# Kernel tuning notes

Measured on AMD Instinct MI355X. Metric: run time of the kernel, lower is better.

Reference implementation:

```python
import jax, jax.numpy as jnp
import numpy as np

B, S, F, D, H, L = 32768, 32, 10, 64, 4, 2
HD = D // H  # head_dim = 16
DFF = 2 * D  # ffn hidden = 128
DH = D // 2  # head hidden = 32


def _ln(x, g, b, eps=1e-5):
    mu = jnp.mean(x, axis=-1, keepdims=True)
    var = jnp.mean((x - mu) ** 2, axis=-1, keepdims=True)
    return (x - mu) * jax.lax.rsqrt(var + eps) * g + b


def setup_inputs() -> dict:
    key = jax.random.key(0)
    ks = jax.random.split(key, 16)
    r = lambda k, shp, s=0.05: jax.random.normal(k, shp, dtype=jnp.float32) * s
    return {
        "x": jax.random.normal(ks[0], (B, S, F), dtype=jnp.float32),
        "w_in": r(ks[1], (F, D)), "b_in": jnp.zeros((D,), jnp.float32),
        "pos": r(ks[2], (S, D)),
        "wq": r(ks[3], (L, D, D)), "wk": r(ks[4], (L, D, D)), "wv": r(ks[5], (L, D, D)),
        "wo": r(ks[6], (L, D, D)), "bo": jnp.zeros((L, D), jnp.float32),
        "g1": jnp.ones((L, D), jnp.float32), "be1": jnp.zeros((L, D), jnp.float32),
        "g2": jnp.ones((L, D), jnp.float32), "be2": jnp.zeros((L, D), jnp.float32),
        "w1": r(ks[7], (L, D, DFF)), "b1": jnp.zeros((L, DFF), jnp.float32),
        "w2": r(ks[8], (L, DFF, D)), "b2": jnp.zeros((L, D), jnp.float32),
        "hw1": r(ks[9], (D, DH)), "hb1": jnp.zeros((DH,), jnp.float32),
        "hw2": r(ks[10], (DH, 1)), "hb2": jnp.zeros((1,), jnp.float32),
    }


def reference(x, w_in, b_in, pos, wq, wk, wv, wo, bo, g1, be1, g2, be2,
              w1, b1, w2, b2, hw1, hb1, hw2, hb2):
    b, s, _ = x.shape
    h = x @ w_in + b_in + pos[None, :s]  # [B,S,D]
    scale = 1.0 / np.sqrt(HD)
    for i in range(L):
        # --- attention sublayer (pre-LN) ---
        hn = _ln(h, g1[i], be1[i])
        q = (hn @ wq[i]).reshape(b, s, H, HD)
        k = (hn @ wk[i]).reshape(b, s, H, HD)
        v = (hn @ wv[i]).reshape(b, s, H, HD)
        scores = jnp.einsum('bqhd,bkhd->bhqk', q, k) * scale
        attn = jax.nn.softmax(scores, axis=-1)
        ctx = jnp.einsum('bhqk,bkhd->bqhd', attn, v).reshape(b, s, D)
        h = h + ctx @ wo[i] + bo[i]
        # --- FFN sublayer (pre-LN) ---
        hn = _ln(h, g2[i], be2[i])
        h = h + jax.nn.relu(hn @ w1[i] + b1[i]) @ w2[i] + b2[i]
    pooled = h.mean(axis=1)  # [B,D]
    out = jax.nn.relu(pooled @ hw1 + hb1) @ hw2 + hb2
    return jnp.tanh(out)  # [B,1]
```

## Files before the change

### kernel.cpp

```cpp
#include <hip/hip_runtime.h>
#include <cmath>

typedef _Float16 h8_t __attribute__((ext_vector_type(8)));
typedef float f4_t __attribute__((ext_vector_type(4)));

constexpr int Bsz = 32768, S = 32, F = 10, Dm = 64, Ln = 2, DFF = 128;
constexpr int ZP = 72;
constexpr int VP = 40;
constexpr int NB = 2;

constexpr int ZONE_H = S * ZP;
constexpr int VT_H   = Dm * VP;
constexpr int SMEM_H = NB * (ZONE_H + VT_H);

constexpr int NFRAG = 4 + Ln * 64;
constexpr size_t PB_OFF = (size_t)NFRAG * 512 * 2;

__global__ __launch_bounds__(256, 2)
void prep_kernel(const float* __restrict__ w_in, const float* __restrict__ b_in,
                 const float* __restrict__ pos,
                 const float* __restrict__ wq, const float* __restrict__ wk,
                 const float* __restrict__ wv, const float* __restrict__ wo,
                 const float* __restrict__ w1, const float* __restrict__ w2,
                 _Float16* __restrict__ wsf, float* __restrict__ pbf) {
  int gid = blockIdx.x * 256 + threadIdx.x;
  int lane = gid & 63;
  int l15 = lane & 15, lk8 = (lane >> 4) << 3;
  if (gid < NFRAG * 64) {
    int frag = gid >> 6;
    float vals[8];
    if (frag < 4) {
      int n = 16 * frag + l15;
      #pragma unroll
      for (int j = 0; j < 8; ++j) {
        int k = lk8 + j;
        vals[j] = (k < F) ? w_in[k * Dm + n] : 0.f;
      }
    } else {
      int f = frag - 4;
      int layer = f >> 6; f &= 63;
      const float* W; int ncols, n, kbase;
      if (f < 32) {
        int sub = f >> 3, g = f & 7;
        int nt = g & 3, kt = g >> 2;
        W = ((sub == 0) ? wk : (sub == 1) ? wv : (sub == 2) ? wq : wo) + layer * Dm * Dm;
        ncols = Dm; n = 16 * nt + l15; kbase = kt * 32 + lk8;
      } else if (f < 48) {
        int g = f - 32, nt = g & 7, kt = g >> 3;
        W = w1 + layer * Dm * DFF; ncols = DFF; n = 16 * nt + l15; kbase = kt * 32 + lk8;
      } else {
        int g = f - 48, nt = g & 3, kt = g >> 2;
        W = w2 + layer * DFF * Dm; ncols = Dm; n = 16 * nt + l15; kbase = kt * 32 + lk8;
      }
      #pragma unroll
      for (int j = 0; j < 8; ++j) vals[j] = W[(kbase + j) * ncols + n];
    }
    h8_t o;
    #pragma unroll
    for (int j = 0; j < 8; ++j) o[j] = (_Float16)vals[j];
    *(h8_t*)&wsf[(size_t)gid * 8] = o;
  } else if (gid < NFRAG * 64 + 8 * 64) {
    int r = gid - NFRAG * 64;
    int pb = r >> 6;
    int mt = pb >> 2, nt = pb & 3;
    int row = 16 * mt + ((lane >> 4) << 2);
    int col = 16 * nt + l15;
    f4_t v;
    #pragma unroll
    for (int q = 0; q < 4; ++q) v[q] = pos[(row + q) * Dm + col] + b_in[col];
    *(f4_t*)&pbf[(size_t)r * 4] = v;
  }
}

__global__ __launch_bounds__(128, 4)
void tlob_kernel(const float* __restrict__ x,
                 const float* __restrict__ g1, const float* __restrict__ be1,
                 const float* __restrict__ g2, const float* __restrict__ be2,
                 const float* __restrict__ bo, const float* __restrict__ b1,
                 const float* __restrict__ b2, const float* __restrict__ hw1,
                 const float* __restrict__ hb1, const float* __restrict__ hw2,
                 const float* __restrict__ hb2,
                 const _Float16* __restrict__ wsf, const float* __restrict__ pbf,
                 float* __restrict__ out) {
  __shared__ __align__(16) _Float16 smem[SMEM_H];
  const int tid = threadIdx.x;
  const int lane = tid & 63;
  const int wid = tid >> 6;
  const int elem = blockIdx.x * NB + wid;

  _Float16* zone = smem + wid * ZONE_H;
  _Float16* vT = smem + NB * ZONE_H + wid * VT_H;

  const int l15 = lane & 15;
  const int G = lane >> 4;
  const int lk8 = G << 3;
  const int r0b = G << 2;
  const int swzR = ((l15 >> 2) & 3) << 3;
  int col4[4];
  #pragma unroll
  for (int nt = 0; nt < 4; ++nt) col4[nt] = l15 + 16 * nt;

  const h8_t* FR = (const h8_t*)wsf;
  auto ldf = [&](int f) -> h8_t { return FR[f * 64 + lane]; };

  f4_t z4; z4[0] = 0.f; z4[1] = 0.f; z4[2] = 0.f; z4[3] = 0.f;
  h8_t hz;
  #pragma unroll
  for (int j = 0; j < 8; ++j) hz[j] = (_Float16)0.f;

  auto mfma = [&](h8_t a, h8_t b, f4_t c) -> f4_t {
    return __builtin_amdgcn_mfma_f32_16x16x32_f16(a, b, c, 0, 0, 0);
  };
  auto cstore = [&](_Float16* buf, int pitch, int mt, int col, f4_t v, float scale) {
    int c = col ^ lk8;
    int r = 16 * mt + r0b;
    #pragma unroll
    for (int q = 0; q < 4; ++q) buf[(r + q) * pitch + c] = (_Float16)(v[q] * scale);
  };
  auto zfrag = [&](int i1, int i2) -> h8_t {
    return *(const h8_t*)&zone[(l15 + 16 * i1) * ZP + ((i2 * 32 + lk8) ^ swzR)];
  };

  h8_t xa[2];
  #pragma unroll
  for (int mt = 0; mt < 2; ++mt) {
    const float* xr = x + (size_t)elem * (S * F) + (16 * mt + l15) * F;
    h8_t v = hz;
    #pragma unroll
    for (int j = 0; j < 8; ++j) {
      int f = lk8 + j;
      if (f < F) v[j] = (_Float16)xr[f];
    }
    xa[mt] = v;
  }

  f4_t hacc[2][4];
  #pragma unroll
  for (int nt = 0; nt < 4; ++nt) {
    h8_t wb = ldf(nt);
    #pragma unroll
    for (int mt = 0; mt < 2; ++mt) {
      f4_t ini = *(const f4_t*)&pbf[((size_t)(mt * 4 + nt) * 64 + lane) * 4];
      hacc[mt][nt] = mfma(xa[mt], wb, ini);
    }
  }

  auto doLN = [&](const float* g, const float* be, h8_t fr[2][2]) {
    float gv[4], bv[4];
    #pragma unroll
    for (int nt = 0; nt < 4; ++nt) { gv[nt] = g[col4[nt]]; bv[nt] = be[col4[nt]]; }
    #pragma unroll
    for (int mt = 0; mt < 2; ++mt) {
      f4_t ps = hacc[mt][0] + hacc[mt][1] + hacc[mt][2] + hacc[mt][3];
      f4_t pq = hacc[mt][0] * hacc[mt][0] + hacc[mt][1] * hacc[mt][1] +
                hacc[mt][2] * hacc[mt][2] + hacc[mt][3] * hacc[mt][3];
      #pragma unroll
      for (int m = 1; m <= 8; m <<= 1) {
        #pragma unroll
        for (int q = 0; q < 4; ++q) {
          ps[q] += __shfl_xor(ps[q], m);
          pq[q] += __shfl_xor(pq[q], m);
        }
      }
      f4_t muv, rsv;
      #pragma unroll
      for (int q = 0; q < 4; ++q) {
        float mu = ps[q] * (1.f / 64.f);
        float var = pq[q] * (1.f / 64.f) - mu * mu;
        muv[q] = mu; rsv[q] = rsqrtf(var + 1e-5f);
      }
      #pragma unroll
      for (int nt = 0; nt < 4; ++nt) {
        int c = col4[nt] ^ lk8;
        int r = 16 * mt + r0b;
        #pragma unroll
        for (int q = 0; q < 4; ++q) {
          float hn = (hacc[mt][nt][q] - muv[q]) * rsv[q] * gv[nt] + bv[nt];
          zone[(r + q) * ZP + c] = (_Float16)hn;
        }
      }
    }
    #pragma unroll
    for (int i1 = 0; i1 < 2; ++i1)
      #pragma unroll
      for (int i2 = 0; i2 < 2; ++i2) fr[i1][i2] = zfrag(i1, i2);
  };

  #pragma unroll 1
  for (int layer = 0; layer < Ln; ++layer) {
    const int fb = 4 + layer * 64;
    float bov[4];
    #pragma unroll
    for (int nt = 0; nt < 4; ++nt) bov[nt] = bo[layer * Dm + col4[nt]];

    h8_t hnf[2][2];
    doLN(g1 + layer * Dm, be1 + layer * Dm, hnf);

    h8_t kA[2][2];
    {
      #pragma unroll
      for (int nt = 0; nt < 4; ++nt) {
        h8_t w0 = ldf(fb + 0 + 0 * 4 + nt), w1f = ldf(fb + 0 + 1 * 4 + nt);
        #pragma unroll
        for (int mt = 0; mt < 2; ++mt) {
          f4_t acc = mfma(hnf[mt][0], w0, z4);
          acc = mfma(hnf[mt][1], w1f, acc);
          cstore(zone, ZP, mt, col4[nt], acc, 1.f);
        }
      }
      #pragma unroll
      for (int i1 = 0; i1 < 2; ++i1)
        #pragma unroll
        for (int i2 = 0; i2 < 2; ++i2) kA[i1][i2] = zfrag(i1, i2);
    }

    #pragma unroll
    for (int mtd = 0; mtd < 4; ++mtd) {
      h8_t a0 = ldf(fb + 8 + 0 * 4 + mtd), a1 = ldf(fb + 8 + 1 * 4 + mtd);
      #pragma unroll
      for (int nts = 0; nts < 2; ++nts) {
        f4_t acc = mfma(a0, hnf[nts][0], z4);
        acc = mfma(a1, hnf[nts][1], acc);
        cstore(vT, VP, mtd, l15 + 16 * nts, acc, 1.f);
      }
    }

    h8_t qf[2][2];
    {
      #pragma unroll
      for (int nt = 0; nt < 4; ++nt) {
        h8_t w0 = ldf(fb + 16 + 0 * 4 + nt), w1f = ldf(fb + 16 + 1 * 4 + nt);
        #pragma unroll
        for (int mt = 0; mt < 2; ++mt) {
          f4_t acc = mfma(hnf[mt][0], w0, z4);
          acc = mfma(hnf[mt][1], w1f, acc);
          cstore(zone, ZP, mt, col4[nt], acc, 0.25f);
        }
      }
      #pragma unroll
      for (int i1 = 0; i1 < 2; ++i1)
        #pragma unroll
        for (int i2 = 0; i2 < 2; ++i2) qf[i1][i2] = zfrag(i1, i2);
    }

    f4_t ctxf[2][4];
    #pragma unroll
    for (int hd = 0; hd < 4; ++hd) {
      const int kt = hd >> 1;
      bool keep = ((hd & 1) == 0) ? (lane < 32) : (lane >= 32);
      h8_t a0 = keep ? kA[0][kt] : hz;
      h8_t a1 = keep ? kA[1][kt] : hz;
      f4_t p[2][2];
      #pragma unroll
      for (int nq = 0; nq < 2; ++nq) {
        p[0][nq] = mfma(a0, qf[nq][kt], z4);
        p[1][nq] = mfma(a1, qf[nq][kt], z4);
      }
      #pragma unroll
      for (int nq = 0; nq < 2; ++nq) {
        #pragma unroll
        for (int mk = 0; mk < 2; ++mk)
          #pragma unroll
          for (int q = 0; q < 4; ++q) p[mk][nq][q] = __expf(p[mk][nq][q]);
        f4_t s4 = p[0][nq] + p[1][nq];
        float sm = s4[0] + s4[1] + s4[2] + s4[3];
        sm += __shfl_xor(sm, 16);
        sm += __shfl_xor(sm, 32);
        float inv = __builtin_amdgcn_rcpf(sm);
        #pragma unroll
        for (int mk = 0; mk < 2; ++mk)
          #pragma unroll
          for (int q = 0; q < 4; ++q) p[mk][nq][q] *= inv;
      }
      #pragma unroll
      for (int nq = 0; nq < 2; ++nq)
        #pragma unroll
        for (int mk = 0; mk < 2; ++mk)
          #pragma unroll
          for (int q = 0; q < 4; ++q)
            zone[(16 * nq + l15) * ZP + ((16 * mk + r0b + q) ^ swzR)] =
                (_Float16)p[mk][nq][q];
      h8_t pA0 = zfrag(0, 0), pA1 = zfrag(1, 0);
      h8_t vB = *(const h8_t*)&vT[(hd * 16 + l15) * VP + (lk8 ^ swzR)];
      ctxf[0][hd] = mfma(pA0, vB, z4);
      ctxf[1][hd] = mfma(pA1, vB, z4);
    }

    #pragma unroll
    for (int mt = 0; mt < 2; ++mt)
      #pragma unroll
      for (int hd = 0; hd < 4; ++hd) cstore(zone, ZP, mt, col4[hd], ctxf[mt][hd], 1.f);
    h8_t ca[2][2];
    #pragma unroll
    for (int i1 = 0; i1 < 2; ++i1)
      #pragma unroll
      for (int i2 = 0; i2 < 2; ++i2) ca[i1][i2] = zfrag(i1, i2);
    #pragma unroll
    for (int nt = 0; nt < 4; ++nt) {
      h8_t w0 = ldf(fb + 24 + 0 * 4 + nt), w1f = ldf(fb + 24 + 1 * 4 + nt);
      #pragma unroll
      for (int mt = 0; mt < 2; ++mt) {
        f4_t acc = mfma(ca[mt][0], w0, hacc[mt][nt]);
        acc = mfma(ca[mt][1], w1f, acc);
        #pragma unroll
        for (int q = 0; q < 4; ++q) hacc[mt][nt][q] = acc[q] + bov[nt];
      }
    }

    h8_t hn2f[2][2];
    doLN(g2 + layer * Dm, be2 + layer * Dm, hn2f);
    #pragma unroll 1
    for (int hf = 0; hf < 2; ++hf) {
      #pragma unroll
      for (int ntl = 0; ntl < 4; ++ntl) {
        int ntg = hf * 4 + ntl;
        h8_t w0 = ldf(fb + 32 + 0 * 8 + ntg), w1f = ldf(fb + 32 + 1 * 8 + ntg);
        float b1v = b1[layer * DFF + hf * 64 + col4[ntl]];
        f4_t bb; bb[0] = b1v; bb[1] = b1v; bb[2] = b1v; bb[3] = b1v;
        #pragma unroll
        for (int mt = 0; mt < 2; ++mt) {
          f4_t acc = mfma(hn2f[mt][0], w0, bb);
          acc = mfma(hn2f[mt][1], w1f, acc);
          #pragma unroll
          for (int q = 0; q < 4; ++q) acc[q] = fmaxf(acc[q], 0.f);
          cstore(zone, ZP, mt, col4[ntl], acc, 1.f);
        }
      }
      h8_t rf[2][2];
      #pragma unroll
      for (int i1 = 0; i1 < 2; ++i1)
        #pragma unroll
        for (int i2 = 0; i2 < 2; ++i2) rf[i1][i2] = zfrag(i1, i2);
      #pragma unroll
      for (int nt = 0; nt < 4; ++nt) {
        h8_t w0 = ldf(fb + 48 + (hf * 2 + 0) * 4 + nt);
        h8_t w1f = ldf(fb + 48 + (hf * 2 + 1) * 4 + nt);
        #pragma unroll
        for (int mt = 0; mt < 2; ++mt) {
          f4_t acc = mfma(rf[mt][0], w0, hacc[mt][nt]);
          hacc[mt][nt] = mfma(rf[mt][1], w1f, acc);
        }
      }
    }
    #pragma unroll
    for (int mt = 0; mt < 2; ++mt)
      #pragma unroll
      for (int nt = 0; nt < 4; ++nt) {
        float b2v = b2[layer * Dm + col4[nt]];
        #pragma unroll
        for (int q = 0; q < 4; ++q) hacc[mt][nt][q] += b2v;
      }
  }

  {
    float* pf = (float*)zone;
    #pragma unroll
    for (int nt = 0; nt < 4; ++nt) {
      float s = 0.f;
      #pragma unroll
      for (int mt = 0; mt < 2; ++mt)
        #pragma unroll
        for (int q = 0; q < 4; ++q) s += hacc[mt][nt][q];
      s += __shfl_xor(s, 16);
      s += __shfl_xor(s, 32);
      pf[col4[nt]] = s * (1.f / 32.f);
    }
    int j = lane & 31;
    float r = hb1[j];
    #pragma unroll
    for (int dd = 0; dd < 64; ++dd) r = fmaf(pf[dd], hw1[dd * 32 + j], r);
    r = fmaxf(r, 0.f);
    float t = r * hw2[j];
    t += __shfl_xor(t, 1); t += __shfl_xor(t, 2); t += __shfl_xor(t, 4);
    t += __shfl_xor(t, 8); t += __shfl_xor(t, 16);
    if (lane == 0) out[elem] = tanhf(t + hb2[0]);
  }
}

extern "C" void kernel_launch(void* const* d_in, const int* in_sizes, int n_in,
                              void* d_out, int out_size, void* d_ws, size_t ws_size,
                              hipStream_t stream) {
  (void)in_sizes; (void)n_in; (void)ws_size; (void)out_size;
  const float* x    = (const float*)d_in[0];
  const float* w_in = (const float*)d_in[1];
  const float* b_in = (const float*)d_in[2];
  const float* pos  = (const float*)d_in[3];
  const float* wq   = (const float*)d_in[4];
  const float* wk   = (const float*)d_in[5];
  const float* wv   = (const float*)d_in[6];
  const float* wo   = (const float*)d_in[7];
  const float* bo   = (const float*)d_in[8];
  const float* g1   = (const float*)d_in[9];
  const float* be1  = (const float*)d_in[10];
  const float* g2   = (const float*)d_in[11];
  const float* be2  = (const float*)d_in[12];
  const float* w1   = (const float*)d_in[13];
  const float* b1   = (const float*)d_in[14];
  const float* w2   = (const float*)d_in[15];
  const float* b2   = (const float*)d_in[16];
  const float* hw1  = (const float*)d_in[17];
  const float* hb1  = (const float*)d_in[18];
  const float* hw2  = (const float*)d_in[19];
  const float* hb2  = (const float*)d_in[20];
  float* out = (float*)d_out;

  _Float16* wsf = (_Float16*)d_ws;
  float* pbf = (float*)((char*)d_ws + PB_OFF);

  hipLaunchKernelGGL(prep_kernel, dim3(35), dim3(256), 0, stream,
                     w_in, b_in, pos, wq, wk, wv, wo, w1, w2, wsf, pbf);
  hipLaunchKernelGGL(tlob_kernel, dim3(Bsz / NB), dim3(128), 0, stream,
                     x, g1, be1, g2, be2, bo, b1, b2, hw1, hb1, hw2, hb2,
                     (const _Float16*)wsf, (const float*)pbf, out);
}
```

Before: 564.5 us.

## Stream attention heads from shared memory and store context per head to cut registers

Attention no longer keeps the Q fragments and all four heads' context accumulators in registers. Q fragments are read from shared memory per key tile, and each head's context goes straight to shared memory. Probabilities are staged in a separate per-wave buffer so they no longer overwrite Q in the zone. Lambdas become forceinline device functions, and launch bounds drop from 4 to 3 blocks per CU, presumably to relieve register pressure and spilling at the cost of fewer resident waves.

```diff
diff --git a/kernel.cpp b/kernel.cpp
--- a/kernel.cpp
+++ b/kernel.cpp
@@ -11,7 +11,8 @@
 
 constexpr int ZONE_H = S * ZP;
 constexpr int VT_H   = Dm * VP;
-constexpr int SMEM_H = NB * (ZONE_H + VT_H);
+constexpr int PB_H   = S * VP;
+constexpr int SMEM_H = NB * (ZONE_H + VT_H + PB_H);
 
 constexpr int NFRAG = 4 + Ln * 64;
 constexpr size_t PB_OFF = (size_t)NFRAG * 512 * 2;
@@ -72,7 +73,75 @@
   }
 }
 
-__global__ __launch_bounds__(128, 4)
+__device__ __forceinline__ f4_t mfma16(h8_t a, h8_t b, f4_t c) {
+  return __builtin_amdgcn_mfma_f32_16x16x32_f16(a, b, c, 0, 0, 0);
+}
+__device__ __forceinline__ void cstore(_Float16* buf, int pitch, int mt, int col,
+                                       f4_t v, float scale, int lk8, int r0b) {
+  int c = col ^ lk8;
+  int r = 16 * mt + r0b;
+  #pragma unroll
+  for (int q = 0; q < 4; ++q) buf[(r + q) * pitch + c] = (_Float16)(v[q] * scale);
+}
+__device__ __forceinline__ h8_t zfrag(const _Float16* zone, int i1, int i2,
+                                      int l15, int lk8, int swzR) {
+  return *(const h8_t*)&zone[(l15 + 16 * i1) * ZP + ((i2 * 32 + lk8) ^ swzR)];
+}
+__device__ __forceinline__ h8_t vpfrag(const _Float16* buf, int row,
+                                       int lk8, int swzR) {
+  return *(const h8_t*)&buf[row * VP + (lk8 ^ swzR)];
+}
+
+struct Frag22 { h8_t f[2][2]; };
+
+__device__ __forceinline__ Frag22 doLN(const f4_t (&hacc)[2][4],
+                                       const float* __restrict__ g,
+                                       const float* __restrict__ be,
+                                       _Float16* zone, int l15, int lk8,
+                                       int r0b, int swzR) {
+  float gv[4], bv[4];
+  #pragma unroll
+  for (int nt = 0; nt < 4; ++nt) { gv[nt] = g[l15 + 16 * nt]; bv[nt] = be[l15 + 16 * nt]; }
+  #pragma unroll
+  for (int mt = 0; mt < 2; ++mt) {
+    f4_t ps = hacc[mt][0] + hacc[mt][1] + hacc[mt][2] + hacc[mt][3];
+    f4_t pq = hacc[mt][0] * hacc[mt][0] + hacc[mt][1] * hacc[mt][1] +
+              hacc[mt][2] * hacc[mt][2] + hacc[mt][3] * hacc[mt][3];
+    #pragma unroll
+    for (int m = 1; m <= 8; m <<= 1) {
+      #pragma unroll
+      for (int q = 0; q < 4; ++q) {
+        ps[q] += __shfl_xor(ps[q], m);
+        pq[q] += __shfl_xor(pq[q], m);
+      }
+    }
+    f4_t muv, rsv;
+    #pragma unroll
+    for (int q = 0; q < 4; ++q) {
+      float mu = ps[q] * (1.f / 64.f);
+      float var = pq[q] * (1.f / 64.f) - mu * mu;
+      muv[q] = mu; rsv[q] = rsqrtf(var + 1e-5f);
+    }
+    #pragma unroll
+    for (int nt = 0; nt < 4; ++nt) {
+      int c = (l15 + 16 * nt) ^ lk8;
+      int r = 16 * mt + r0b;
+      #pragma unroll
+      for (int q = 0; q < 4; ++q) {
+        float hn = (hacc[mt][nt][q] - muv[q]) * rsv[q] * gv[nt] + bv[nt];
+        zone[(r + q) * ZP + c] = (_Float16)hn;
+      }
+    }
+  }
+  Frag22 out;
+  #pragma unroll
+  for (int i1 = 0; i1 < 2; ++i1)
+    #pragma unroll
+    for (int i2 = 0; i2 < 2; ++i2) out.f[i1][i2] = zfrag(zone, i1, i2, l15, lk8, swzR);
+  return out;
+}
+
+__global__ __launch_bounds__(128, 3)
 void tlob_kernel(const float* __restrict__ x,
                  const float* __restrict__ g1, const float* __restrict__ be1,
                  const float* __restrict__ g2, const float* __restrict__ be2,
@@ -89,37 +158,21 @@
   const int elem = blockIdx.x * NB + wid;
 
   _Float16* zone = smem + wid * ZONE_H;
-  _Float16* vT = smem + NB * ZONE_H + wid * VT_H;
+  _Float16* vT   = smem + NB * ZONE_H + wid * VT_H;
+  _Float16* pb   = smem + NB * (ZONE_H + VT_H) + wid * PB_H;
 
   const int l15 = lane & 15;
   const int G = lane >> 4;
   const int lk8 = G << 3;
   const int r0b = G << 2;
   const int swzR = ((l15 >> 2) & 3) << 3;
-  int col4[4];
-  #pragma unroll
-  for (int nt = 0; nt < 4; ++nt) col4[nt] = l15 + 16 * nt;
 
   const h8_t* FR = (const h8_t*)wsf;
-  auto ldf = [&](int f) -> h8_t { return FR[f * 64 + lane]; };
 
   f4_t z4; z4[0] = 0.f; z4[1] = 0.f; z4[2] = 0.f; z4[3] = 0.f;
   h8_t hz;
   #pragma unroll
   for (int j = 0; j < 8; ++j) hz[j] = (_Float16)0.f;
-
-  auto mfma = [&](h8_t a, h8_t b, f4_t c) -> f4_t {
-    return __builtin_amdgcn_mfma_f32_16x16x32_f16(a, b, c, 0, 0, 0);
-  };
-  auto cstore = [&](_Float16* buf, int pitch, int mt, int col, f4_t v, float scale) {
-    int c = col ^ lk8;
-    int r = 16 * mt + r0b;
-    #pragma unroll
-    for (int q = 0; q < 4; ++q) buf[(r + q) * pitch + c] = (_Float16)(v[q] * scale);
-  };
-  auto zfrag = [&](int i1, int i2) -> h8_t {
-    return *(const h8_t*)&zone[(l15 + 16 * i1) * ZP + ((i2 * 32 + lk8) ^ swzR)];
-  };
 
   h8_t xa[2];
   #pragma unroll
@@ -137,208 +190,161 @@
   f4_t hacc[2][4];
   #pragma unroll
   for (int nt = 0; nt < 4; ++nt) {
-    h8_t wb = ldf(nt);
+    h8_t wb = FR[nt * 64 + lane];
     #pragma unroll
     for (int mt = 0; mt < 2; ++mt) {
       f4_t ini = *(const f4_t*)&pbf[((size_t)(mt * 4 + nt) * 64 + lane) * 4];
-      hacc[mt][nt] = mfma(xa[mt], wb, ini);
-    }
-  }
-
-  auto doLN = [&](const float* g, const float* be, h8_t fr[2][2]) {
-    float gv[4], bv[4];
-    #pragma unroll
-    for (int nt = 0; nt < 4; ++nt) { gv[nt] = g[col4[nt]]; bv[nt] = be[col4[nt]]; }
-    #pragma unroll
-    for (int mt = 0; mt < 2; ++mt) {
-      f4_t ps = hacc[mt][0] + hacc[mt][1] + hacc[mt][2] + hacc[mt][3];
-      f4_t pq = hacc[mt][0] * hacc[mt][0] + hacc[mt][1] * hacc[mt][1] +
-                hacc[mt][2] * hacc[mt][2] + hacc[mt][3] * hacc[mt][3];
-      #pragma unroll
-      for (int m = 1; m <= 8; m <<= 1) {
-        #pragma unroll
-        for (int q = 0; q < 4; ++q) {
-          ps[q] += __shfl_xor(ps[q], m);
-          pq[q] += __shfl_xor(pq[q], m);
-        }
-      }
-      f4_t muv, rsv;
-      #pragma unroll
-      for (int q = 0; q < 4; ++q) {
-        float mu = ps[q] * (1.f / 64.f);
-        float var = pq[q] * (1.f / 64.f) - mu * mu;
-        muv[q] = mu; rsv[q] = rsqrtf(var + 1e-5f);
-      }
-      #pragma unroll
-      for (int nt = 0; nt < 4; ++nt) {
-        int c = col4[nt] ^ lk8;
-        int r = 16 * mt + r0b;
-        #pragma unroll
-        for (int q = 0; q < 4; ++q) {
-          float hn = (hacc[mt][nt][q] - muv[q]) * rsv[q] * gv[nt] + bv[nt];
-          zone[(r + q) * ZP + c] = (_Float16)hn;
-        }
-      }
-    }
-    #pragma unroll
-    for (int i1 = 0; i1 < 2; ++i1)
-      #pragma unroll
-      for (int i2 = 0; i2 < 2; ++i2) fr[i1][i2] = zfrag(i1, i2);
-  };
+      hacc[mt][nt] = mfma16(xa[mt], wb, ini);
+    }
+  }
 
   #pragma unroll 1
   for (int layer = 0; layer < Ln; ++layer) {
     const int fb = 4 + layer * 64;
-    float bov[4];
-    #pragma unroll
-    for (int nt = 0; nt < 4; ++nt) bov[nt] = bo[layer * Dm + col4[nt]];
-
-    h8_t hnf[2][2];
-    doLN(g1 + layer * Dm, be1 + layer * Dm, hnf);
+
+    Frag22 hnf = doLN(hacc, g1 + layer * Dm, be1 + layer * Dm,
+                      zone, l15, lk8, r0b, swzR);
 
     h8_t kA[2][2];
+    #pragma unroll
+    for (int nt = 0; nt < 4; ++nt) {
+      h8_t w0 = FR[(fb + nt) * 64 + lane], w1f = FR[(fb + 4 + nt) * 64 + lane];
+      #pragma unroll
+      for (int mt = 0; mt < 2; ++mt) {
+        f4_t acc = mfma16(hnf.f[mt][0], w0, z4);
+        acc = mfma16(hnf.f[mt][1], w1f, acc);
+        cstore(zone, ZP, mt, l15 + 16 * nt, acc, 1.f, lk8, r0b);
+      }
+    }
+    #pragma unroll
+    for (int i1 = 0; i1 < 2; ++i1)
+      #pragma unroll
+      for (int i2 = 0; i2 < 2; ++i2) kA[i1][i2] = zfrag(zone, i1, i2, l15, lk8, swzR);
+
+    #pragma unroll
+    for (int mtd = 0; mtd < 4; ++mtd) {
+      h8_t a0 = FR[(fb + 8 + mtd) * 64 + lane], a1 = FR[(fb + 12 + mtd) * 64 + lane];
+      #pragma unroll
+      for (int nts = 0; nts < 2; ++nts) {
+        f4_t acc = mfma16(a0, hnf.f[nts][0], z4);
+        acc = mfma16(a1, hnf.f[nts][1], acc);
+        cstore(vT, VP, mtd, l15 + 16 * nts, acc, 1.f, lk8, r0b);
+      }
+    }
+
+    #pragma unroll
+    for (int nt = 0; nt < 4; ++nt) {
+      h8_t w0 = FR[(fb + 16 + nt) * 64 + lane], w1f = FR[(fb + 20 + nt) * 64 + lane];
+      #pragma unroll
+      for (int mt = 0; mt < 2; ++mt) {
+        f4_t acc = mfma16(hnf.f[mt][0], w0, z4);
+        acc = mfma16(hnf.f[mt][1], w1f, acc);
+        cstore(zone, ZP, mt, l15 + 16 * nt, acc, 0.25f, lk8, r0b);
+      }
+    }
+
+    #pragma unroll
+    for (int kt = 0; kt < 2; ++kt) {
+      h8_t qp0 = zfrag(zone, 0, kt, l15, lk8, swzR);
+      h8_t qp1 = zfrag(zone, 1, kt, l15, lk8, swzR);
+      #pragma unroll
+      for (int sub = 0; sub < 2; ++sub) {
+        const int hd = 2 * kt + sub;
+        bool keep = (sub == 0) ? (lane < 32) : (lane >= 32);
+        h8_t a0 = keep ? kA[0][kt] : hz;
+        h8_t a1 = keep ? kA[1][kt] : hz;
+        f4_t p[2][2];
+        p[0][0] = mfma16(a0, qp0, z4);
+        p[0][1] = mfma16(a0, qp1, z4);
+        p[1][0] = mfma16(a1, qp0, z4);
+        p[1][1] = mfma16(a1, qp1, z4);
+        #pragma unroll
+        for (int nq = 0; nq < 2; ++nq) {
+          #pragma unroll
+          for (int mk = 0; mk < 2; ++mk)
+            #pragma unroll
+            for (int q = 0; q < 4; ++q) p[mk][nq][q] = __expf(p[mk][nq][q]);
+          f4_t s4 = p[0][nq] + p[1][nq];
+          float sm = s4[0] + s4[1] + s4[2] + s4[3];
+          sm += __shfl_xor(sm, 16);
+          sm += __shfl_xor(sm, 32);
+          float inv = __builtin_amdgcn_rcpf(sm);
+          #pragma unroll
+          for (int mk = 0; mk < 2; ++mk)
+            #pragma unroll
+            for (int q = 0; q < 4; ++q) p[mk][nq][q] *= inv;
+        }
+        #pragma unroll
+        for (int nq = 0; nq < 2; ++nq)
+          #pragma unroll
+          for (int mk = 0; mk < 2; ++mk)
+            #pragma unroll
+            for (int q = 0; q < 4; ++q)
+              pb[(16 * nq + l15) * VP + ((16 * mk + r0b + q) ^ swzR)] =
+                  (_Float16)p[mk][nq][q];
+        h8_t pA0 = vpfrag(pb, l15, lk8, swzR);
+        h8_t pA1 = vpfrag(pb, l15 + 16, lk8, swzR);
+        h8_t vB = vpfrag(vT, hd * 16 + l15, lk8, swzR);
+        f4_t c0 = mfma16(pA0, vB, z4);
+        f4_t c1 = mfma16(pA1, vB, z4);
+        cstore(zone, ZP, 0, l15 + 16 * hd, c0, 1.f, lk8, r0b);
+        cstore(zone, ZP, 1, l15 + 16 * hd, c1, 1.f, lk8, r0b);
+      }
+    }
+
     {
+      h8_t ca[2][2];
+      #pragma unroll
+      for (int i1 = 0; i1 < 2; ++i1)
+        #pragma unroll
+        for (int i2 = 0; i2 < 2; ++i2) ca[i1][i2] = zfrag(zone, i1, i2, l15, lk8, swzR);
       #pragma unroll
       for (int nt = 0; nt < 4; ++nt) {
-        h8_t w0 = ldf(fb + 0 + 0 * 4 + nt), w1f = ldf(fb + 0 + 1 * 4 + nt);
+        h8_t w0 = FR[(fb + 24 + nt) * 64 + lane], w1f = FR[(fb + 28 + nt) * 64 + lane];
+        float bov = bo[layer * Dm + l15 + 16 * nt];
         #pragma unroll
         for (int mt = 0; mt < 2; ++mt) {
-          f4_t acc = mfma(hnf[mt][0], w0, z4);
-          acc = mfma(hnf[mt][1], w1f, acc);
-          cstore(zone, ZP, mt, col4[nt], acc, 1.f);
+          f4_t acc = mfma16(ca[mt][0], w0, hacc[mt][nt]);
+          acc = mfma16(ca[mt][1], w1f, acc);
+          #pragma unroll
+          for (int q = 0; q < 4; ++q) hacc[mt][nt][q] = acc[q] + bov;
         }
       }
-      #pragma unroll
-      for (int i1 = 0; i1 < 2; ++i1)
-        #pragma unroll
-        for (int i2 = 0; i2 < 2; ++i2) kA[i1][i2] = zfrag(i1, i2);
-    }
-
-    #pragma unroll
-    for (int mtd = 0; mtd < 4; ++mtd) {
-      h8_t a0 = ldf(fb + 8 + 0 * 4 + mtd), a1 = ldf(fb + 8 + 1 * 4 + mtd);
-      #pragma unroll
-      for (int nts = 0; nts < 2; ++nts) {
-        f4_t acc = mfma(a0, hnf[nts][0], z4);
-        acc = mfma(a1, hnf[nts][1], acc);
-        cstore(vT, VP, mtd, l15 + 16 * nts, acc, 1.f);
-      }
-    }
-
-    h8_t qf[2][2];
-    {
-      #pragma unroll
-      for (int nt = 0; nt < 4; ++nt) {
-        h8_t w0 = ldf(fb + 16 + 0 * 4 + nt), w1f = ldf(fb + 16 + 1 * 4 + nt);
-        #pragma unroll
-        for (int mt = 0; mt < 2; ++mt) {
-          f4_t acc = mfma(hnf[mt][0], w0, z4);
-          acc = mfma(hnf[mt][1], w1f, acc);
-          cstore(zone, ZP, mt, col4[nt], acc, 0.25f);
-        }
-      }
-      #pragma unroll
-      for (int i1 = 0; i1 < 2; ++i1)
-        #pragma unroll
-        for (int i2 = 0; i2 < 2; ++i2) qf[i1][i2] = zfrag(i1, i2);
-    }
-
-    f4_t ctxf[2][4];
-    #pragma unroll
-    for (int hd = 0; hd < 4; ++hd) {
-      const int kt = hd >> 1;
-      bool keep = ((hd & 1) == 0) ? (lane < 32) : (lane >= 32);
-      h8_t a0 = keep ? kA[0][kt] : hz;
-      h8_t a1 = keep ? kA[1][kt] : hz;
-      f4_t p[2][2];
-      #pragma unroll
-      for (int nq = 0; nq < 2; ++nq) {
-        p[0][nq] = mfma(a0, qf[nq][kt], z4);
-        p[1][nq] = mfma(a1, qf[nq][kt], z4);
-      }
-      #pragma unroll
-      for (int nq = 0; nq < 2; ++nq) {
-        #pragma unroll
-        for (int mk = 0; mk < 2; ++mk)
-          #pragma unroll
-          for (int q = 0; q < 4; ++q) p[mk][nq][q] = __expf(p[mk][nq][q]);
-        f4_t s4 = p[0][nq] + p[1][nq];
-        float sm = s4[0] + s4[1] + s4[2] + s4[3];
-        sm += __shfl_xor(sm, 16);
-        sm += __shfl_xor(sm, 32);
-        float inv = __builtin_amdgcn_rcpf(sm);
-        #pragma unroll
-        for (int mk = 0; mk < 2; ++mk)
-          #pragma unroll
-          for (int q = 0; q < 4; ++q) p[mk][nq][q] *= inv;
-      }
-      #pragma unroll
-      for (int nq = 0; nq < 2; ++nq)
-        #pragma unroll
-        for (int mk = 0; mk < 2; ++mk)
-          #pragma unroll
-          for (int q = 0; q < 4; ++q)
-            zone[(16 * nq + l15) * ZP + ((16 * mk + r0b + q) ^ swzR)] =
-                (_Float16)p[mk][nq][q];
-      h8_t pA0 = zfrag(0, 0), pA1 = zfrag(1, 0);
-      h8_t vB = *(const h8_t*)&vT[(hd * 16 + l15) * VP + (lk8 ^ swzR)];
-      ctxf[0][hd] = mfma(pA0, vB, z4);
-      ctxf[1][hd] = mfma(pA1, vB, z4);
-    }
-
-    #pragma unroll
-    for (int mt = 0; mt < 2; ++mt)
-      #pragma unroll
-      for (int hd = 0; hd < 4; ++hd) cstore(zone, ZP, mt, col4[hd], ctxf[mt][hd], 1.f);
-    h8_t ca[2][2];
-    #pragma unroll
-    for (int i1 = 0; i1 < 2; ++i1)
-      #pragma unroll
-      for (int i2 = 0; i2 < 2; ++i2) ca[i1][i2] = zfrag(i1, i2);
-    #pragma unroll
-    for (int nt = 0; nt < 4; ++nt) {
-      h8_t w0 = ldf(fb + 24 + 0 * 4 + nt), w1f = ldf(fb + 24 + 1 * 4 + nt);
-      #pragma unroll
-      for (int mt = 0; mt < 2; ++mt) {
-        f4_t acc = mfma(ca[mt][0], w0, hacc[mt][nt]);
-        acc = mfma(ca[mt][1], w1f, acc);
-        #pragma unroll
-        for (int q = 0; q < 4; ++q) hacc[mt][nt][q] = acc[q] + bov[nt];
-      }
-    }
-
-    h8_t hn2f[2][2];
-    doLN(g2 + layer * Dm, be2 + layer * Dm, hn2f);
+    }
+
+    Frag22 hn2f = doLN(hacc, g2 + layer * Dm, be2 + layer * Dm,
+                       zone, l15, lk8, r0b, swzR);
     #pragma unroll 1
     for (int hf = 0; hf < 2; ++hf) {
       #pragma unroll
       for (int ntl = 0; ntl < 4; ++ntl) {
         int ntg = hf * 4 + ntl;
-        h8_t w0 = ldf(fb + 32 + 0 * 8 + ntg), w1f = ldf(fb + 32 + 1 * 8 + ntg);
-        float b1v = b1[layer * DFF + hf * 64 + col4[ntl]];
+        h8_t w0 = FR[(fb + 32 + ntg) * 64 + lane];
+        h8_t w1f = FR[(fb + 40 + ntg) * 64 + lane];
+        float b1v = b1[layer * DFF + hf * 64 + l15 + 16 * ntl];
         f4_t bb; bb[0] = b1v; bb[1] = b1v; bb[2] = b1v; bb[3] = b1v;
         #pragma unroll
         for (int mt = 0; mt < 2; ++mt) {
-          f4_t acc = mfma(hn2f[mt][0], w0, bb);
-          acc = mfma(hn2f[mt][1], w1f, acc);
+          f4_t acc = mfma16(hn2f.f[mt][0], w0, bb);
+          acc = mfma16(hn2f.f[mt][1], w1f, acc);
           #pragma unroll
           for (int q = 0; q < 4; ++q) acc[q] = fmaxf(acc[q], 0.f);
-          cstore(zone, ZP, mt, col4[ntl], acc, 1.f);
+          cstore(zone, ZP, mt, l15 + 16 * ntl, acc, 1.f, lk8, r0b);
         }
       }
       h8_t rf[2][2];
       #pragma unroll
       for (int i1 = 0; i1 < 2; ++i1)
         #pragma unroll
-        for (int i2 = 0; i2 < 2; ++i2) rf[i1][i2] = zfrag(i1, i2);
+        for (int i2 = 0; i2 < 2; ++i2) rf[i1][i2] = zfrag(zone, i1, i2, l15, lk8, swzR);
       #pragma unroll
       for (int nt = 0; nt < 4; ++nt) {
-        h8_t w0 = ldf(fb + 48 + (hf * 2 + 0) * 4 + nt);
-        h8_t w1f = ldf(fb + 48 + (hf * 2 + 1) * 4 + nt);
+        h8_t w0 = FR[(fb + 48 + (hf * 2 + 0) * 4 + nt) * 64 + lane];
+        h8_t w1f = FR[(fb + 48 + (hf * 2 + 1) * 4 + nt) * 64 + lane];
         #pragma unroll
         for (int mt = 0; mt < 2; ++mt) {
-          f4_t acc = mfma(rf[mt][0], w0, hacc[mt][nt]);
-          hacc[mt][nt] = mfma(rf[mt][1], w1f, acc);
+          f4_t acc = mfma16(rf[mt][0], w0, hacc[mt][nt]);
+          hacc[mt][nt] = mfma16(rf[mt][1], w1f, acc);
         }
       }
     }
@@ -346,7 +352,7 @@
     for (int mt = 0; mt < 2; ++mt)
       #pragma unroll
       for (int nt = 0; nt < 4; ++nt) {
-        float b2v = b2[layer * Dm + col4[nt]];
+        float b2v = b2[layer * Dm + l15 + 16 * nt];
         #pragma unroll
         for (int q = 0; q < 4; ++q) hacc[mt][nt][q] += b2v;
       }
@@ -363,7 +369,7 @@
         for (int q = 0; q < 4; ++q) s += hacc[mt][nt][q];
       s += __shfl_xor(s, 16);
       s += __shfl_xor(s, 32);
-      pf[col4[nt]] = s * (1.f / 32.f);
+      pf[l15 + 16 * nt] = s * (1.f / 32.f);
     }
     int j = lane & 31;
     float r = hb1[j];
```

Result: faster. 494.7 us (-12.4%).
